# Kernel optimization log

Measured on AMD Instinct MI355X. Metric: run time of the kernel, lower is better.

The kernel has to match this reference:

```python
import jax, jax.numpy as jnp
import numpy as np
import math

VOCAB, D, L, B, S = 32000, 1024, 6, 4, 1024
FF = 4 * D


def sinusoidal_pe(max_len, d_model):
    pos = np.arange(max_len)[:, None].astype(np.float32)
    div = np.exp(np.arange(0, d_model, 2).astype(np.float32) * (-math.log(10000.0) / d_model))
    pe = np.zeros((max_len, d_model), dtype=np.float32)
    pe[:, 0::2] = np.sin(pos * div)
    pe[:, 1::2] = np.cos(pos * div)
    return jnp.asarray(pe)


def layernorm(x, g, b, eps=1e-5):
    mu = jnp.mean(x, axis=-1, keepdims=True)
    var = jnp.mean(jnp.square(x - mu), axis=-1, keepdims=True)
    return (x - mu) * jax.lax.rsqrt(var + eps) * g + b


def setup_inputs() -> dict:
    key = jax.random.key(0)
    ks = jax.random.split(key, 16)
    s = 0.02
    inp = {
        "input_ids": jax.random.randint(ks[0], (B, S), 0, VOCAB, dtype=jnp.int32),
        "attention_mask": jnp.ones((B, S), dtype=jnp.int32),
        "emb": jax.random.normal(ks[1], (VOCAB, D), jnp.float32) * s,
        "Wq": jax.random.normal(ks[2], (L, D, D), jnp.float32) * s,
        "Wk": jax.random.normal(ks[3], (L, D, D), jnp.float32) * s,
        "Wv": jax.random.normal(ks[4], (L, D, D), jnp.float32) * s,
        "bq": jnp.zeros((L, D), jnp.float32),
        "bk": jnp.zeros((L, D), jnp.float32),
        "bv": jnp.zeros((L, D), jnp.float32),
        "g1": jnp.ones((L, D), jnp.float32),
        "beta1": jnp.zeros((L, D), jnp.float32),
        "Wf1": jax.random.normal(ks[5], (L, D, FF), jnp.float32) * s,
        "bf1": jnp.zeros((L, FF), jnp.float32),
        "Wf2": jax.random.normal(ks[6], (L, FF, D), jnp.float32) * s,
        "bf2": jnp.zeros((L, D), jnp.float32),
        "g2": jnp.ones((L, D), jnp.float32),
        "beta2": jnp.zeros((L, D), jnp.float32),
    }
    return inp


def reference(input_ids, attention_mask, emb, Wq, Wk, Wv, bq, bk, bv,
              g1, beta1, Wf1, bf1, Wf2, bf2, g2, beta2):
    pe = sinusoidal_pe(1024, D)
    x = emb[input_ids] + pe[: input_ids.shape[1]]           # [B,S,D]
    mask = (attention_mask[:, None, :] != 0)                # [B,1,S]
    scale = 1.0 / math.sqrt(D)
    for l in range(L):
        Q = jnp.einsum('bsd,de->bse', x, Wq[l]) + bq[l]
        K = jnp.einsum('bsd,de->bse', x, Wk[l]) + bk[l]
        V = jnp.einsum('bsd,de->bse', x, Wv[l]) + bv[l]
        scores = jnp.einsum('bqd,bkd->bqk', Q, K) * scale   # [B,S,S]
        scores = jnp.where(mask, scores, -1e9)
        attn = jax.nn.softmax(scores, axis=-1)
        a = jnp.einsum('bqk,bkd->bqd', attn, V)
        x = layernorm(x + a, g1[l], beta1[l])
        h = jax.nn.relu(jnp.einsum('bsd,df->bsf', x, Wf1[l]) + bf1[l])
        f = jnp.einsum('bsf,fd->bsd', h, Wf2[l]) + bf2[l]
        x = layernorm(x + f, g2[l], beta2[l])
    return x
```

## Files before the change

### kernel.cpp

```cpp
#include <hip/hip_runtime.h>

typedef __bf16 bf16_t;
typedef __bf16 bf16x8 __attribute__((ext_vector_type(8)));
typedef float f32x4 __attribute__((ext_vector_type(4)));
typedef float f32x16 __attribute__((ext_vector_type(16)));
typedef unsigned short u16;

#define DEV static __device__ __forceinline__

DEV float bf2f(u16 u) { __bf16 h = __builtin_bit_cast(__bf16, u); return (float)h; }
DEV u16 f2bf(float f) { __bf16 h = (__bf16)f; return __builtin_bit_cast(u16, h); }

DEV void gll16(bf16_t* lds, const bf16_t* g) {
    __builtin_amdgcn_global_load_lds(
        (const __attribute__((address_space(1))) void*)g,
        (__attribute__((address_space(3))) void*)lds, 16, 0, 0);
}

#define WAITV(N) asm volatile("s_waitcnt vmcnt(" #N ")" ::: "memory")

template <int EPI>
__global__ __launch_bounds__(512, 1)
void gemm8p(const bf16_t* __restrict__ A, int lda,
            const bf16_t* __restrict__ Bt, int ldb,
            bf16_t* __restrict__ C, int ldc,
            const float* __restrict__ bias, int K,
            long kadv, long cadv)
{
    __shared__ bf16_t Asm[2 * 2 * 8192];
    __shared__ bf16_t Bsm[2 * 2 * 8192];
    const int tid = threadIdx.x, w = tid >> 6, l = tid & 63;
    const int z = blockIdx.z;
    A  += (size_t)z * kadv;
    Bt += (size_t)z * kadv;
    C  += (size_t)z * cadv;

    const int gx = gridDim.x;
    int lin = blockIdx.y * gx + blockIdx.x;
    const int nlin = gx * gridDim.y;
    lin = (lin & 7) * (nlin >> 3) + (lin >> 3);
    const size_t row0 = (size_t)(lin / gx) * 256;
    const size_t col0 = (size_t)(lin % gx) * 256;

    const int wr = w >> 2, wc = w & 3;
    const int bh = wc >> 1;
    const int browoff = (wc & 1) * 64;
    const int r32 = l & 31, hk = l >> 5, sw = l & 7;

    const int srow = w * 8 + (l >> 3);
    const int sslot8 = ((l & 7) ^ ((l >> 3) & 7)) * 8;
    const bf16_t* AgH0 = A  + (row0 + srow) * (size_t)lda + sslot8;
    const bf16_t* BgH0 = Bt + (col0 + srow) * (size_t)ldb + sslot8;
    const size_t a128 = (size_t)128 * lda, b128 = (size_t)128 * ldb;
    const size_t a64  = (size_t)64 * lda,  b64  = (size_t)64 * ldb;
    const int wlds = w * 512;

#define STAGE_PAIR(buf, tt, p)                                                 \
    do {                                                                       \
        const int koff = (tt) * 64;                                            \
        if ((p) == 0) {                                                        \
            gll16(Asm + ((buf)*2+0)*8192 + wlds,        AgH0 + koff);          \
            gll16(Asm + ((buf)*2+0)*8192 + 4096 + wlds, AgH0 + koff + a64);    \
        } else if ((p) == 1) {                                                 \
            gll16(Asm + ((buf)*2+1)*8192 + wlds,        AgH0 + a128 + koff);   \
            gll16(Asm + ((buf)*2+1)*8192 + 4096 + wlds, AgH0 + a128 + koff + a64); \
        } else if ((p) == 2) {                                                 \
            gll16(Bsm + ((buf)*2+0)*8192 + wlds,        BgH0 + koff);          \
            gll16(Bsm + ((buf)*2+0)*8192 + 4096 + wlds, BgH0 + koff + b64);    \
        } else {                                                               \
            gll16(Bsm + ((buf)*2+1)*8192 + wlds,        BgH0 + b128 + koff);   \
            gll16(Bsm + ((buf)*2+1)*8192 + 4096 + wlds, BgH0 + b128 + koff + b64); \
        }                                                                      \
    } while (0)

    f32x16 acc[4][2] = {};
    const int NT = K >> 6;

    STAGE_PAIR(0, 0, 0); STAGE_PAIR(0, 0, 1); STAGE_PAIR(0, 0, 2); STAGE_PAIR(0, 0, 3);
    if (NT > 1) { STAGE_PAIR(1, 1, 0); WAITV(2); } else { WAITV(0); }
    __builtin_amdgcn_sched_barrier(0);
    __builtin_amdgcn_s_barrier();

    for (int t = 0; t < NT; ++t) {
        const int cur = t & 1, nxt = cur ^ 1;
        const bool hasN1 = (t + 1 < NT), hasN2 = (t + 2 < NT);
        const bf16_t* Ab = Asm + (cur * 2 + wr) * 8192;
        const bf16_t* Bb = Bsm + (cur * 2 + bh) * 8192;

        bf16x8 bR[2][4], aR[2][4];
#pragma unroll
        for (int ni = 0; ni < 2; ni++)
#pragma unroll
            for (int ks = 0; ks < 4; ks++)
                bR[ni][ks] = *(const bf16x8*)&Bb[(browoff + ni * 32 + r32) * 64 + ((ks * 2 + hk) ^ sw) * 8];
#pragma unroll
        for (int mi = 0; mi < 2; mi++)
#pragma unroll
            for (int ks = 0; ks < 4; ks++)
                aR[mi][ks] = *(const bf16x8*)&Ab[(mi * 32 + r32) * 64 + ((ks * 2 + hk) ^ sw) * 8];
        if (hasN1) { STAGE_PAIR(nxt, t + 1, 1); STAGE_PAIR(nxt, t + 1, 2); }
        __builtin_amdgcn_s_setprio(1);
#pragma unroll
        for (int mi = 0; mi < 2; mi++)
#pragma unroll
            for (int ni = 0; ni < 2; ni++)
#pragma unroll
                for (int ks = 0; ks < 4; ks++)
                    acc[mi][ni] = __builtin_amdgcn_mfma_f32_32x32x16_bf16(aR[mi][ks], bR[ni][ks], acc[mi][ni], 0, 0, 0);
        __builtin_amdgcn_s_setprio(0);

        bf16x8 a2[2][4];
#pragma unroll
        for (int mi = 0; mi < 2; mi++)
#pragma unroll
            for (int ks = 0; ks < 4; ks++)
                a2[mi][ks] = *(const bf16x8*)&Ab[((2 + mi) * 32 + r32) * 64 + ((ks * 2 + hk) ^ sw) * 8];
        if (hasN1) STAGE_PAIR(nxt, t + 1, 3);
        __builtin_amdgcn_s_setprio(1);
#pragma unroll
        for (int mi = 0; mi < 2; mi++)
#pragma unroll
            for (int ni = 0; ni < 2; ni++)
#pragma unroll
                for (int ks = 0; ks < 4; ks++)
                    acc[2 + mi][ni] = __builtin_amdgcn_mfma_f32_32x32x16_bf16(a2[mi][ks], bR[ni][ks], acc[2 + mi][ni], 0, 0, 0);
        __builtin_amdgcn_s_setprio(0);

        __builtin_amdgcn_s_barrier();
        if (hasN2) STAGE_PAIR(cur, t + 2, 0);
        if (hasN1) {
            if (hasN2) { WAITV(2); } else { WAITV(0); }
            __builtin_amdgcn_sched_barrier(0);
        }
        __builtin_amdgcn_s_barrier();
    }
#undef STAGE_PAIR

#pragma unroll
    for (int ni = 0; ni < 2; ni++) {
        size_t c = col0 + wc * 64 + ni * 32 + r32;
        float bv = bias ? bias[c] : 0.f;
#pragma unroll
        for (int mi = 0; mi < 4; mi++) {
            size_t rb = row0 + wr * 128 + mi * 32 + hk * 4;
#pragma unroll
            for (int reg = 0; reg < 16; reg++) {
                size_t r = rb + (reg & 3) + 8 * (reg >> 2);
                float v = acc[mi][ni][reg] + bv;
                if (EPI == 1) v = fmaxf(v, 0.f);
                C[r * ldc + c] = (bf16_t)v;
            }
        }
    }
}

template <int EPI>
__global__ __launch_bounds__(256)
void gemm_db(const bf16_t* __restrict__ A, int lda, long sA,
             const bf16_t* __restrict__ Bt, int ldb, long sB,
             void* __restrict__ Cv, int ldc, long sC,
             const float* __restrict__ bias, int K, float scale)
{
    __shared__ bf16_t Asm[2][128 * 64];
    __shared__ bf16_t Bsm[2][128 * 64];
    const int tid = threadIdx.x, w = tid >> 6, l = tid & 63;
    const int bz = blockIdx.z;

    const int gx = gridDim.x;
    int lin = blockIdx.y * gx + blockIdx.x;
    const int nlin = gx * gridDim.y;
    lin = (lin & 7) * (nlin >> 3) + (lin >> 3);
    const size_t row0 = (size_t)(lin / gx) * 128;
    const size_t col0 = (size_t)(lin % gx) * 128;

    A  += (size_t)bz * sA;
    Bt += (size_t)bz * sB;

    const int lr = l >> 3;
    const int sl = (l & 7) ^ lr;
    const bf16_t* Ag = A  + (row0 + (size_t)(w * 32) + lr) * lda + sl * 8;
    const bf16_t* Bg = Bt + (col0 + (size_t)(w * 32) + lr) * ldb + sl * 8;
    const int wlds = (w * 32) * 64;

#define STA(buf, tt)                                                           \
    do { const int ko = (tt) * 64;                                             \
        _Pragma("unroll")                                                      \
        for (int c = 0; c < 4; c++)                                            \
            gll16(&Asm[buf][wlds + c * 8 * 64], Ag + (size_t)(c * 8) * lda + ko); \
    } while (0)
#define STB(buf, tt)                                                           \
    do { const int ko = (tt) * 64;                                             \
        _Pragma("unroll")                                                      \
        for (int c = 0; c < 4; c++)                                            \
            gll16(&Bsm[buf][wlds + c * 8 * 64], Bg + (size_t)(c * 8) * ldb + ko); \
    } while (0)

    const int wm = (w >> 1) * 64, wn = (w & 1) * 64;
    const int r32 = l & 31, hk = l >> 5, sw = l & 7;
    f32x16 acc[2][2] = {};
    const int NT = K >> 6;

    STA(0, 0); STB(0, 0);
    if (NT > 1) { STA(1, 1); WAITV(4); } else { WAITV(0); }
    __builtin_amdgcn_sched_barrier(0);
    __builtin_amdgcn_s_barrier();

    for (int t = 0; t < NT; ++t) {
        const int cur = t & 1, nxt = cur ^ 1;
        const bool hasN1 = (t + 1 < NT), hasN2 = (t + 2 < NT);

        bf16x8 a0[2][2], b0[2][2];
#pragma unroll
        for (int i = 0; i < 2; i++)
#pragma unroll
            for (int ks = 0; ks < 2; ks++) {
                a0[i][ks] = *(const bf16x8*)&Asm[cur][(wm + i * 32 + r32) * 64 + ((ks * 2 + hk) ^ sw) * 8];
                b0[i][ks] = *(const bf16x8*)&Bsm[cur][(wn + i * 32 + r32) * 64 + ((ks * 2 + hk) ^ sw) * 8];
            }
        if (hasN1) STB(nxt, t + 1);
        __builtin_amdgcn_s_setprio(1);
#pragma unroll
        for (int mi = 0; mi < 2; mi++)
#pragma unroll
            for (int ni = 0; ni < 2; ni++)
#pragma unroll
                for (int ks = 0; ks < 2; ks++)
                    acc[mi][ni] = __builtin_amdgcn_mfma_f32_32x32x16_bf16(a0[mi][ks], b0[ni][ks], acc[mi][ni], 0, 0, 0);
        __builtin_amdgcn_s_setprio(0);

        bf16x8 a1[2][2], b1[2][2];
#pragma unroll
        for (int i = 0; i < 2; i++)
#pragma unroll
            for (int ks = 0; ks < 2; ks++) {
                a1[i][ks] = *(const bf16x8*)&Asm[cur][(wm + i * 32 + r32) * 64 + (((2 + ks) * 2 + hk) ^ sw) * 8];
                b1[i][ks] = *(const bf16x8*)&Bsm[cur][(wn + i * 32 + r32) * 64 + (((2 + ks) * 2 + hk) ^ sw) * 8];
            }
        __builtin_amdgcn_s_setprio(1);
#pragma unroll
        for (int mi = 0; mi < 2; mi++)
#pragma unroll
            for (int ni = 0; ni < 2; ni++)
#pragma unroll
                for (int ks = 0; ks < 2; ks++)
                    acc[mi][ni] = __builtin_amdgcn_mfma_f32_32x32x16_bf16(a1[mi][ks], b1[ni][ks], acc[mi][ni], 0, 0, 0);
        __builtin_amdgcn_s_setprio(0);

        __builtin_amdgcn_s_barrier();
        if (hasN2) STA(cur, t + 2);
        if (hasN1) {
            if (hasN2) { WAITV(4); } else { WAITV(0); }
            __builtin_amdgcn_sched_barrier(0);
        }
        __builtin_amdgcn_s_barrier();
    }
#undef STA
#undef STB

#pragma unroll
    for (int ni = 0; ni < 2; ni++) {
        size_t c = col0 + wn + ni * 32 + r32;
        float bv = (EPI == 0 || EPI == 1) ? (bias ? bias[c] : 0.f) : 0.f;
#pragma unroll
        for (int mi = 0; mi < 2; mi++) {
            size_t rb = row0 + wm + mi * 32 + hk * 4;
#pragma unroll
            for (int reg = 0; reg < 16; reg++) {
                size_t r = rb + (reg & 3) + 8 * (reg >> 2);
                float v = acc[mi][ni][reg];
                if (EPI == 2) {
                    ((float*)Cv + (size_t)bz * sC)[r * ldc + c] = v * scale;
                } else if (EPI == 3) {
                    ((bf16_t*)Cv + (size_t)bz * sC)[r * ldc + c] = (bf16_t)(v * scale);
                } else {
                    v += bv;
                    if (EPI == 1) v = fmaxf(v, 0.f);
                    ((bf16_t*)Cv + (size_t)bz * sC)[r * ldc + c] = (bf16_t)v;
                }
            }
        }
    }
}

__global__ __launch_bounds__(256)
void prep_kernel(const float* __restrict__ Wq, const float* __restrict__ Wk,
                 const float* __restrict__ Wv, const float* __restrict__ Wf1,
                 const float* __restrict__ Wf2,
                 const float* __restrict__ bq, const float* __restrict__ bk,
                 const float* __restrict__ bv,
                 const int* __restrict__ ids, const float* __restrict__ emb,
                 bf16_t* __restrict__ wqkvTA, bf16_t* __restrict__ wf1TA,
                 bf16_t* __restrict__ wf2TA, float* __restrict__ qbiasA,
                 bf16_t* __restrict__ xb)
{
    __shared__ bf16_t tls[4][64 * 64];
    const size_t DD = 1024 * 1024;
    int id = blockIdx.x;
    if (id < 4224) {
        const float* src; bf16_t* dst; int ldin, ldout, bx, by;
        if (id < 1152) {
            int layer = id / 192, r = id % 192, which = r >> 6, t = r & 63;
            src = (which == 0 ? Wq : which == 1 ? Wk : Wv) + (size_t)layer * DD;
            dst = wqkvTA + (size_t)layer * 3 * DD + (size_t)which * DD;
            ldin = 1024; ldout = 1024; bx = (t & 15) * 64; by = (t >> 4) * 256;
        } else if (id < 2688) {
            int i = id - 1152, layer = i >> 8, t = i & 255;
            src = Wf1 + (size_t)layer * 4 * DD; dst = wf1TA + (size_t)layer * 4 * DD;
            ldin = 4096; ldout = 1024; bx = (t & 63) * 64; by = (t >> 6) * 256;
        } else {
            int i = id - 2688, layer = i >> 8, t = i & 255;
            src = Wf2 + (size_t)layer * 4 * DD; dst = wf2TA + (size_t)layer * 4 * DD;
            ldin = 1024; ldout = 4096; bx = (t & 15) * 64; by = (t >> 4) * 256;
        }
        const int tid = threadIdx.x;
        const int cg = tid & 15, ri = tid >> 4;
#pragma unroll
        for (int sub = 0; sub < 4; sub++) {
#pragma unroll
            for (int k = 0; k < 4; k++) {
                int r = ri + k * 16;
                float4 v = *(const float4*)&src[(size_t)(by + sub * 64 + r) * ldin + bx + cg * 4];
                ushort4 o = {f2bf(v.x), f2bf(v.y), f2bf(v.z), f2bf(v.w)};
                int g = (cg ^ ((r >> 2) & 15) ^ sub) & 15;
                *(ushort4*)&tls[sub][r * 64 + g * 4] = o;
            }
        }
        __syncthreads();
        const int c = tid & 31, sub = c >> 3, j = c & 7;
#pragma unroll
        for (int p = 0; p < 8; p++) {
            int i = p * 8 + (tid >> 5);
            u16 vals[8];
#pragma unroll
            for (int m = 0; m < 8; m++) {
                int rr = j * 8 + m;
                int gg = ((i >> 2) ^ (rr >> 2) ^ sub) & 15;
                vals[m] = __builtin_bit_cast(u16, tls[sub][rr * 64 + gg * 4 + (i & 3)]);
            }
            uint4 ov;
            ov.x = (unsigned)vals[0] | ((unsigned)vals[1] << 16);
            ov.y = (unsigned)vals[2] | ((unsigned)vals[3] << 16);
            ov.z = (unsigned)vals[4] | ((unsigned)vals[5] << 16);
            ov.w = (unsigned)vals[6] | ((unsigned)vals[7] << 16);
            *(uint4*)&dst[(size_t)(bx + i) * ldout + by + c * 8] = ov;
        }
        return;
    }
    id -= 4224;
    if (id < 72) {
        int i = id * 256 + threadIdx.x;
        int lyr = i / 3072, j = i - lyr * 3072;
        qbiasA[i] = (j < 1024) ? bq[lyr * 1024 + j]
                  : (j < 2048) ? bk[lyr * 1024 + j - 1024]
                               : bv[lyr * 1024 + j - 2048];
        return;
    }
    id -= 72;
    const int row = id;
    const int s = row & 1023;
    const int eid = ids[row];
    const float* er = emb + (size_t)eid * 1024;
    bf16_t* br = xb + (size_t)row * 1024;
#pragma unroll
    for (int k = 0; k < 2; k++) {
        int i = threadIdx.x + 256 * k;
        int d = 2 * i;
        float dv = expf((float)d * -0.008994473019508f);
        float ph = (float)s * dv;
        float sv, cv;
        sincosf(ph, &sv, &cv);
        float2 ev = *(const float2*)&er[d];
        ushort2 bo = {f2bf(ev.x + sv), f2bf(ev.y + cv)};
        *(ushort2*)&br[d] = bo;
    }
}

__global__ __launch_bounds__(256)
void softvt_kernel(const bf16_t* __restrict__ sc, const int* __restrict__ amask,
                   bf16_t* __restrict__ p, const bf16_t* __restrict__ qkv,
                   bf16_t* __restrict__ vt)
{
    __shared__ bf16_t tls[64][72];
    int bid = blockIdx.x;
    if (bid < 1024) {
        const int row = bid * 4 + (threadIdx.x >> 6);
        const int l = threadIdx.x & 63;
        const int b = row >> 10;
        const bf16_t* s = sc + (size_t)row * 1024;
        const int* m = amask + (size_t)b * 1024;
        float v[16];
        float mx = -3.0e38f;
#pragma unroll
        for (int i = 0; i < 4; i++) {
            int c = 4 * l + 256 * i;
            ushort4 su = *(const ushort4*)&s[c];
            int4 mv = *(const int4*)&m[c];
            v[4 * i + 0] = mv.x ? bf2f(su.x) : -1e9f;
            v[4 * i + 1] = mv.y ? bf2f(su.y) : -1e9f;
            v[4 * i + 2] = mv.z ? bf2f(su.z) : -1e9f;
            v[4 * i + 3] = mv.w ? bf2f(su.w) : -1e9f;
            mx = fmaxf(mx, fmaxf(fmaxf(v[4 * i], v[4 * i + 1]), fmaxf(v[4 * i + 2], v[4 * i + 3])));
        }
#pragma unroll
        for (int o = 32; o; o >>= 1) mx = fmaxf(mx, __shfl_xor(mx, o, 64));
        float sum = 0.f;
#pragma unroll
        for (int i = 0; i < 16; i++) { v[i] = __expf(v[i] - mx); sum += v[i]; }
#pragma unroll
        for (int o = 32; o; o >>= 1) sum += __shfl_xor(sum, o, 64);
        float inv = 1.0f / sum;
#pragma unroll
        for (int i = 0; i < 4; i++) {
            int c = 4 * l + 256 * i;
            ushort4 st;
            st.x = f2bf(v[4 * i + 0] * inv);
            st.y = f2bf(v[4 * i + 1] * inv);
            st.z = f2bf(v[4 * i + 2] * inv);
            st.w = f2bf(v[4 * i + 3] * inv);
            *(ushort4*)&p[(size_t)row * 1024 + c] = st;
        }
        return;
    }
    bid -= 1024;
    const int z = bid >> 8, t = bid & 255;
    const bf16_t* in = qkv + 2048 + (size_t)z * 1024 * 3072;
    bf16_t* out = vt + (size_t)z * 1024 * 1024;
    const int bx = (t & 15) * 64, by = (t >> 4) * 64;
    const int tid = threadIdx.x;
    const int cj = (tid & 15) * 4, ri = tid >> 4;
#pragma unroll
    for (int k = 0; k < 4; k++) {
        int r = ri + k * 16;
        *(ushort4*)&tls[r][cj] = *(const ushort4*)&in[(size_t)(by + r) * 3072 + bx + cj];
    }
    __syncthreads();
#pragma unroll
    for (int k = 0; k < 4; k++) {
        int i2 = ri + k * 16;
        ushort4 o;
        o.x = __builtin_bit_cast(u16, tls[cj + 0][i2]);
        o.y = __builtin_bit_cast(u16, tls[cj + 1][i2]);
        o.z = __builtin_bit_cast(u16, tls[cj + 2][i2]);
        o.w = __builtin_bit_cast(u16, tls[cj + 3][i2]);
        *(ushort4*)&out[(size_t)(bx + i2) * 1024 + by + cj] = o;
    }
}

__global__ __launch_bounds__(256)
void ln_kernel(const bf16_t* __restrict__ xin, const bf16_t* __restrict__ add,
               const float* __restrict__ g, const float* __restrict__ beta,
               bf16_t* __restrict__ out)
{
    __shared__ float red[8];
    const int row = blockIdx.x;
    const int t = threadIdx.x;
    const size_t base = (size_t)row * 1024 + t * 4;
    ushort4 xu = *(const ushort4*)&xin[base];
    ushort4 au = *(const ushort4*)&add[base];
    float tv[4];
    tv[0] = bf2f(xu.x) + bf2f(au.x);
    tv[1] = bf2f(xu.y) + bf2f(au.y);
    tv[2] = bf2f(xu.z) + bf2f(au.z);
    tv[3] = bf2f(xu.w) + bf2f(au.w);
    float s = tv[0] + tv[1] + tv[2] + tv[3];
    float s2 = tv[0] * tv[0] + tv[1] * tv[1] + tv[2] * tv[2] + tv[3] * tv[3];
#pragma unroll
    for (int o = 32; o; o >>= 1) { s += __shfl_xor(s, o, 64); s2 += __shfl_xor(s2, o, 64); }
    if ((t & 63) == 0) { red[t >> 6] = s; red[4 + (t >> 6)] = s2; }
    __syncthreads();
    s = red[0] + red[1] + red[2] + red[3];
    s2 = red[4] + red[5] + red[6] + red[7];
    const float mu = s * (1.f / 1024.f);
    const float var = s2 * (1.f / 1024.f) - mu * mu;
    const float rs = rsqrtf(var + 1e-5f);
    float4 gu = *(const float4*)&g[t * 4];
    float4 bu = *(const float4*)&beta[t * 4];
    ushort4 ob;
    ob.x = f2bf((tv[0] - mu) * rs * gu.x + bu.x);
    ob.y = f2bf((tv[1] - mu) * rs * gu.y + bu.y);
    ob.z = f2bf((tv[2] - mu) * rs * gu.z + bu.z);
    ob.w = f2bf((tv[3] - mu) * rs * gu.w + bu.w);
    *(ushort4*)&out[base] = ob;
}

template <int F32OUT>
__global__ __launch_bounds__(256)
void ln4_kernel(const bf16_t* __restrict__ xin, const bf16_t* __restrict__ p,
                long pstride, const float* __restrict__ fbias,
                const float* __restrict__ g, const float* __restrict__ beta,
                void* __restrict__ outv)
{
    __shared__ float red[8];
    const int row = blockIdx.x;
    const int t = threadIdx.x;
    const size_t base = (size_t)row * 1024 + t * 4;
    ushort4 xu = *(const ushort4*)&xin[base];
    float4 bb = *(const float4*)&fbias[t * 4];
    float tv[4] = {bf2f(xu.x) + bb.x, bf2f(xu.y) + bb.y,
                   bf2f(xu.z) + bb.z, bf2f(xu.w) + bb.w};
#pragma unroll
    for (int z = 0; z < 4; z++) {
        ushort4 au = *(const ushort4*)&p[(size_t)z * pstride + base];
        tv[0] += bf2f(au.x); tv[1] += bf2f(au.y);
        tv[2] += bf2f(au.z); tv[3] += bf2f(au.w);
    }
    float s = tv[0] + tv[1] + tv[2] + tv[3];
    float s2 = tv[0] * tv[0] + tv[1] * tv[1] + tv[2] * tv[2] + tv[3] * tv[3];
#pragma unroll
    for (int o = 32; o; o >>= 1) { s += __shfl_xor(s, o, 64); s2 += __shfl_xor(s2, o, 64); }
    if ((t & 63) == 0) { red[t >> 6] = s; red[4 + (t >> 6)] = s2; }
    __syncthreads();
    s = red[0] + red[1] + red[2] + red[3];
    s2 = red[4] + red[5] + red[6] + red[7];
    const float mu = s * (1.f / 1024.f);
    const float var = s2 * (1.f / 1024.f) - mu * mu;
    const float rs = rsqrtf(var + 1e-5f);
    float4 gu = *(const float4*)&g[t * 4];
    float4 bu = *(const float4*)&beta[t * 4];
    float y0 = (tv[0] - mu) * rs * gu.x + bu.x;
    float y1 = (tv[1] - mu) * rs * gu.y + bu.y;
    float y2 = (tv[2] - mu) * rs * gu.z + bu.z;
    float y3 = (tv[3] - mu) * rs * gu.w + bu.w;
    if (F32OUT) {
        float4 yo = {y0, y1, y2, y3};
        *(float4*)&((float*)outv)[base] = yo;
    } else {
        ushort4 ob = {f2bf(y0), f2bf(y1), f2bf(y2), f2bf(y3)};
        *(ushort4*)&((bf16_t*)outv)[base] = ob;
    }
}


extern "C" void kernel_launch(void* const* d_in, const int* in_sizes, int n_in,
                              void* d_out, int out_size, void* d_ws, size_t ws_size,
                              hipStream_t stream)
{
    const int*   ids = (const int*)d_in[0];
    const int*   am  = (const int*)d_in[1];
    const float* emb = (const float*)d_in[2];
    const float* Wq  = (const float*)d_in[3];
    const float* Wk  = (const float*)d_in[4];
    const float* Wv  = (const float*)d_in[5];
    const float* bq  = (const float*)d_in[6];
    const float* bk  = (const float*)d_in[7];
    const float* bv  = (const float*)d_in[8];
    const float* g1  = (const float*)d_in[9];
    const float* be1 = (const float*)d_in[10];
    const float* Wf1 = (const float*)d_in[11];
    const float* bf1 = (const float*)d_in[12];
    const float* Wf2 = (const float*)d_in[13];
    const float* bf2_ = (const float*)d_in[14];
    const float* g2  = (const float*)d_in[15];
    const float* be2 = (const float*)d_in[16];

    char* ws = (char*)d_ws;
    bf16_t* xb     = (bf16_t*)(ws + (16LL << 20));
    bf16_t* qkv    = (bf16_t*)(ws + (24LL << 20));
    bf16_t* vt     = (bf16_t*)(ws + (48LL << 20));
    bf16_t* fpart  = (bf16_t*)(ws + (24LL << 20));
    bf16_t* scores = (bf16_t*)(ws + (56LL << 20));
    bf16_t* p      = (bf16_t*)(ws + (72LL << 20));
    bf16_t* h      = (bf16_t*)(ws + (56LL << 20));
    bf16_t* attn   = (bf16_t*)(ws + (88LL << 20));
    bf16_t* wqkvTA = (bf16_t*)(ws + (96LL << 20));
    bf16_t* wf1TA  = (bf16_t*)(ws + (132LL << 20));
    bf16_t* wf2TA  = (bf16_t*)(ws + (180LL << 20));
    float*  qbiasA = (float*)(ws + (228LL << 20));

    const size_t DD = 1024 * 1024;

    prep_kernel<<<8392, 256, 0, stream>>>(Wq, Wk, Wv, Wf1, Wf2, bq, bk, bv,
                                          ids, emb, wqkvTA, wf1TA, wf2TA, qbiasA, xb);

    for (int l = 0; l < 6; l++) {
        gemm8p<0><<<dim3(12, 16, 1), 512, 0, stream>>>(xb, 1024, wqkvTA + (size_t)l * 3 * DD, 1024,
                                                       qkv, 3072, qbiasA + l * 3072, 1024, 0, 0);
        gemm_db<3><<<dim3(8, 8, 4), 256, 0, stream>>>(qkv, 3072, 1024L * 3072,
                                                      qkv + 1024, 3072, 1024L * 3072,
                                                      scores, 1024, 1024L * 1024,
                                                      nullptr, 1024, 0.03125f);
        softvt_kernel<<<2048, 256, 0, stream>>>(scores, am, p, qkv, vt);
        gemm_db<0><<<dim3(8, 8, 4), 256, 0, stream>>>(p, 1024, 1024L * 1024,
                                                      vt, 1024, 1024L * 1024,
                                                      attn, 1024, 1024L * 1024,
                                                      nullptr, 1024, 0.f);
        ln_kernel<<<4096, 256, 0, stream>>>(xb, attn, g1 + l * 1024, be1 + l * 1024, xb);
        gemm8p<1><<<dim3(16, 16, 1), 512, 0, stream>>>(xb, 1024, wf1TA + (size_t)l * 4 * DD, 1024,
                                                       h, 4096, bf1 + l * 4096, 1024, 0, 0);
        gemm8p<0><<<dim3(4, 16, 4), 512, 0, stream>>>(h, 4096, wf2TA + (size_t)l * 4 * DD, 4096,
                                                      fpart, 1024, nullptr, 1024,
                                                      1024, 4096L * 1024);
        if (l == 5)
            ln4_kernel<1><<<4096, 256, 0, stream>>>(xb, fpart, 4096L * 1024, bf2_ + l * 1024,
                                                    g2 + l * 1024, be2 + l * 1024, d_out);
        else
            ln4_kernel<0><<<4096, 256, 0, stream>>>(xb, fpart, 4096L * 1024, bf2_ + l * 1024,
                                                    g2 + l * 1024, be2 + l * 1024, xb);
    }
    (void)in_sizes; (void)n_in; (void)out_size; (void)ws_size;
}
```

Before: 1.176 ms.

## Restructure GEMM main loop into 8-phase ping-pong schedule with finer barriers

Replaces the two-phase per-tile GEMM loop with a manually unrolled two-tile iteration split into four MFMA phases each, separated by workgroup barriers and setprio. LDS fragment reads and global-to-LDS stages are interleaved between the phases, and the wait depth is raised to keep more loads in flight. The aim is to overlap memory traffic with MFMA work more tightly across the 8 waves. It adds many barriers and assumes NT is even and at least 2, since tile 1 is staged unconditionally in the prologue.

```diff
diff --git a/kernel.cpp b/kernel.cpp
--- a/kernel.cpp
+++ b/kernel.cpp
@@ -73,68 +73,82 @@
         }                                                                      \
     } while (0)
 
+#define RD_A(base, half)                                                       \
+    _Pragma("unroll")                                                          \
+    for (int j = 0; j < 2; j++)                                                \
+        _Pragma("unroll")                                                      \
+        for (int ks = 0; ks < 4; ks++)                                         \
+            aF[j][ks] = *(const bf16x8*)&(base)[(((half)*2+j)*32 + r32)*64 + ((ks*2+hk)^sw)*8]
+
+#define RD_B(base, ni, dst)                                                    \
+    _Pragma("unroll")                                                          \
+    for (int ks = 0; ks < 4; ks++)                                             \
+        dst[ks] = *(const bf16x8*)&(base)[(browoff + (ni)*32 + r32)*64 + ((ks*2+hk)^sw)*8]
+
+#define MM(mb, ni, bsrc)                                                       \
+    _Pragma("unroll")                                                          \
+    for (int j = 0; j < 2; j++)                                                \
+        _Pragma("unroll")                                                      \
+        for (int ks = 0; ks < 4; ks++)                                         \
+            acc[(mb)+j][ni] = __builtin_amdgcn_mfma_f32_32x32x16_bf16(aF[j][ks], bsrc[ks], acc[(mb)+j][ni], 0, 0, 0)
+
+#define BAR __builtin_amdgcn_s_barrier()
+#define PRIO1 __builtin_amdgcn_s_setprio(1)
+#define PRIO0 __builtin_amdgcn_s_setprio(0)
+
     f32x16 acc[4][2] = {};
     const int NT = K >> 6;
 
-    STAGE_PAIR(0, 0, 0); STAGE_PAIR(0, 0, 1); STAGE_PAIR(0, 0, 2); STAGE_PAIR(0, 0, 3);
-    if (NT > 1) { STAGE_PAIR(1, 1, 0); WAITV(2); } else { WAITV(0); }
+    STAGE_PAIR(0, 0, 2); STAGE_PAIR(0, 0, 3); STAGE_PAIR(0, 0, 0); STAGE_PAIR(0, 0, 1);
+    STAGE_PAIR(1, 1, 2); STAGE_PAIR(1, 1, 3); STAGE_PAIR(1, 1, 0);
+    WAITV(6);
     __builtin_amdgcn_sched_barrier(0);
-    __builtin_amdgcn_s_barrier();
-
-    for (int t = 0; t < NT; ++t) {
-        const int cur = t & 1, nxt = cur ^ 1;
-        const bool hasN1 = (t + 1 < NT), hasN2 = (t + 2 < NT);
-        const bf16_t* Ab = Asm + (cur * 2 + wr) * 8192;
-        const bf16_t* Bb = Bsm + (cur * 2 + bh) * 8192;
-
-        bf16x8 bR[2][4], aR[2][4];
-#pragma unroll
-        for (int ni = 0; ni < 2; ni++)
-#pragma unroll
-            for (int ks = 0; ks < 4; ks++)
-                bR[ni][ks] = *(const bf16x8*)&Bb[(browoff + ni * 32 + r32) * 64 + ((ks * 2 + hk) ^ sw) * 8];
-#pragma unroll
-        for (int mi = 0; mi < 2; mi++)
-#pragma unroll
-            for (int ks = 0; ks < 4; ks++)
-                aR[mi][ks] = *(const bf16x8*)&Ab[(mi * 32 + r32) * 64 + ((ks * 2 + hk) ^ sw) * 8];
-        if (hasN1) { STAGE_PAIR(nxt, t + 1, 1); STAGE_PAIR(nxt, t + 1, 2); }
-        __builtin_amdgcn_s_setprio(1);
-#pragma unroll
-        for (int mi = 0; mi < 2; mi++)
-#pragma unroll
-            for (int ni = 0; ni < 2; ni++)
-#pragma unroll
-                for (int ks = 0; ks < 4; ks++)
-                    acc[mi][ni] = __builtin_amdgcn_mfma_f32_32x32x16_bf16(aR[mi][ks], bR[ni][ks], acc[mi][ni], 0, 0, 0);
-        __builtin_amdgcn_s_setprio(0);
-
-        bf16x8 a2[2][4];
-#pragma unroll
-        for (int mi = 0; mi < 2; mi++)
-#pragma unroll
-            for (int ks = 0; ks < 4; ks++)
-                a2[mi][ks] = *(const bf16x8*)&Ab[((2 + mi) * 32 + r32) * 64 + ((ks * 2 + hk) ^ sw) * 8];
-        if (hasN1) STAGE_PAIR(nxt, t + 1, 3);
-        __builtin_amdgcn_s_setprio(1);
-#pragma unroll
-        for (int mi = 0; mi < 2; mi++)
-#pragma unroll
-            for (int ni = 0; ni < 2; ni++)
-#pragma unroll
-                for (int ks = 0; ks < 4; ks++)
-                    acc[2 + mi][ni] = __builtin_amdgcn_mfma_f32_32x32x16_bf16(a2[mi][ks], bR[ni][ks], acc[2 + mi][ni], 0, 0, 0);
-        __builtin_amdgcn_s_setprio(0);
-
-        __builtin_amdgcn_s_barrier();
-        if (hasN2) STAGE_PAIR(cur, t + 2, 0);
-        if (hasN1) {
-            if (hasN2) { WAITV(2); } else { WAITV(0); }
-            __builtin_amdgcn_sched_barrier(0);
-        }
-        __builtin_amdgcn_s_barrier();
+    BAR;
+
+    const bf16_t* A0b = Asm + (0 + wr) * 8192;
+    const bf16_t* B0b = Bsm + (0 + bh) * 8192;
+    const bf16_t* A1b = Asm + (2 + wr) * 8192;
+    const bf16_t* B1b = Bsm + (2 + bh) * 8192;
+
+    bf16x8 aF[2][4], bF0[4], bF1[4];
+
+    for (int it = 0; it < (NT >> 1); ++it) {
+        const int t1 = 2 * it + 1, t2 = 2 * it + 2, t3 = 2 * it + 3;
+        const bool h2 = (t2 < NT);
+
+        RD_A(A0b, 0); RD_B(B0b, 0, bF0);
+        STAGE_PAIR(1, t1, 1);
+        BAR; PRIO1; MM(0, 0, bF0); PRIO0; BAR;
+        RD_B(B0b, 1, bF1);
+        BAR; PRIO1; MM(0, 1, bF1); PRIO0; BAR;
+        RD_A(A0b, 1);
+        if (h2) { STAGE_PAIR(0, t2, 2); STAGE_PAIR(0, t2, 3); }
+        BAR; PRIO1; MM(2, 1, bF1); PRIO0; BAR;
+        if (h2) STAGE_PAIR(0, t2, 0);
+        BAR; PRIO1; MM(2, 0, bF0); PRIO0;
+        if (h2) { WAITV(6); } else { WAITV(0); }
+        __builtin_amdgcn_sched_barrier(0);
+        BAR;
+
+        RD_A(A1b, 0); RD_B(B1b, 0, bF0);
+        if (h2) STAGE_PAIR(0, t2, 1);
+        BAR; PRIO1; MM(0, 0, bF0); PRIO0; BAR;
+        RD_B(B1b, 1, bF1);
+        if (h2) STAGE_PAIR(1, t3, 2);
+        BAR; PRIO1; MM(0, 1, bF1); PRIO0; BAR;
+        RD_A(A1b, 1);
+        if (h2) STAGE_PAIR(1, t3, 3);
+        BAR; PRIO1; MM(2, 1, bF1); PRIO0; BAR;
+        if (h2) STAGE_PAIR(1, t3, 0);
+        BAR; PRIO1; MM(2, 0, bF0); PRIO0;
+        if (h2) { WAITV(6); } else { WAITV(0); }
+        __builtin_amdgcn_sched_barrier(0);
+        BAR;
     }
 #undef STAGE_PAIR
+#undef RD_A
+#undef RD_B
+#undef MM
 
 #pragma unroll
     for (int ni = 0; ni < 2; ni++) {
```

After: 1.244 ms. 1.06x slower.
